# Kernel optimization log

Hardware: AMD Instinct MI355X
Metric: run time of the kernel (lower is better)

Reference implementation:

```python
import jax, jax.numpy as jnp
import numpy as np

N_EMBED = 1024
HEAD_SIZE = 128
B, T = 8, 2048


def setup_inputs() -> dict:
    key = jax.random.key(0)
    kx, kk, kq, kv = jax.random.split(key, 4)
    x = jax.random.normal(kx, (B, T, N_EMBED), dtype=jnp.float32)
    Wk = jax.random.normal(kk, (N_EMBED, HEAD_SIZE), dtype=jnp.float32) * (N_EMBED ** -0.5)
    Wq = jax.random.normal(kq, (N_EMBED, HEAD_SIZE), dtype=jnp.float32) * (N_EMBED ** -0.5)
    Wv = jax.random.normal(kv, (N_EMBED, HEAD_SIZE), dtype=jnp.float32) * (N_EMBED ** -0.5)
    return {"x": x, "Wk": Wk, "Wq": Wq, "Wv": Wv}


def reference(x, Wk, Wq, Wv):
    # x: [B, T, C]; single-head causal attention, dropout rate 0 (identity)
    t = x.shape[1]
    k = jnp.einsum("btc,ch->bth", x, Wk)  # keys
    q = jnp.einsum("btc,ch->bth", x, Wq)  # queries
    v = jnp.einsum("btc,ch->bth", x, Wv)  # values
    scale = k.shape[-1] ** -0.5
    scores = jnp.einsum("bqh,bkh->bqk", q, k) * scale  # [B, T, T]
    causal = jnp.tril(jnp.ones((t, t), dtype=bool))
    scores = jnp.where(causal, scores, -jnp.inf)
    attn = jax.nn.softmax(scores, axis=-1)
    return jnp.einsum("bqk,bkh->bqh", attn, v)
```

## Files before the change

### kernel.cpp

```cpp
#include <hip/hip_runtime.h>
#include <hip/hip_bf16.h>
#include <math.h>

#define B_ 8
#define T_ 2048
#define C_ 1024
#define D_ 128
#define M_ (B_*T_)

typedef __attribute__((ext_vector_type(8))) short short8;
typedef __attribute__((ext_vector_type(4))) float floatx4;
typedef __hip_bfloat16 bf16;

#define QSCALE 0.12751744416218247f

#define GLDS16(gsrc, ldst) \
    __builtin_amdgcn_global_load_lds((const __attribute__((address_space(1))) unsigned int*)(gsrc), \
                                     (__attribute__((address_space(3))) unsigned int*)(ldst), 16, 0, 0)

__global__ __launch_bounds__(256) void cvt_w3_kernel(const float* __restrict__ Wq,
                                                     const float* __restrict__ Wk,
                                                     const float* __restrict__ Wv,
                                                     bf16* __restrict__ Wt2) {
    __shared__ bf16 tl[64][136];
    const int t = threadIdx.x;
    const int kc = blockIdx.x, g = blockIdx.y;
    const int k0 = kc * 64;
    const float* W = (g == 0) ? Wq : (g == 1) ? Wk : Wv;
    {
        int k = t >> 2, n0 = (t & 3) * 32;
        const float* src = W + (size_t)(k0 + k) * 128 + n0;
#pragma unroll
        for (int j = 0; j < 4; ++j) {
            float4 v0 = *(const float4*)(src + j * 8);
            float4 v1 = *(const float4*)(src + j * 8 + 4);
            union { short8 s; __hip_bfloat162 h[4]; } u;
            __hip_bfloat162 h;
            h.x = __float2bfloat16(v0.x); h.y = __float2bfloat16(v0.y); u.h[0] = h;
            h.x = __float2bfloat16(v0.z); h.y = __float2bfloat16(v0.w); u.h[1] = h;
            h.x = __float2bfloat16(v1.x); h.y = __float2bfloat16(v1.y); u.h[2] = h;
            h.x = __float2bfloat16(v1.z); h.y = __float2bfloat16(v1.w); u.h[3] = h;
            *(short8*)&tl[k][n0 + j * 8] = u.s;
        }
    }
    __syncthreads();
    {
#pragma unroll
        for (int j = 0; j < 4; ++j) {
            int cid = t + j * 256;
            int lane = cid & 63, dk = (cid >> 6) & 1, cb = cid >> 7;
            int krow = dk * 32 + (lane >> 4) * 8;
            int ncol = cb * 16 + (lane & 15);
            union { short8 s; bf16 e[8]; } u;
#pragma unroll
            for (int e = 0; e < 8; ++e) u.e[e] = tl[krow + e][ncol];
            bf16* dst = Wt2 + ((((size_t)(g * 8 + cb) * 16 + kc) * 2 + dk) * 64 + lane) * 8;
            *(short8*)dst = u.s;
        }
    }
}

__global__ __launch_bounds__(256, 2) void proj12_kernel(const float* __restrict__ x,
                                                        const bf16* __restrict__ Wt2,
                                                        bf16* __restrict__ Qb,
                                                        bf16* __restrict__ Kb,
                                                        bf16* __restrict__ Vt) {
    __shared__ bf16 smem[21504];
    bf16* wlds = smem;
    bf16* xlds = smem + 12288;
    const int t = threadIdx.x;
    const int wave = t >> 6, lane = t & 63;
    const int quad = lane >> 4, l15 = lane & 15;
    const int wr = wave >> 1, wc = wave & 1;
    const int phys = blockIdx.x;
    const int lb = (phys & 7) * 64 + (phys >> 3);
    const int rt = lb >> 1, cg = lb & 1;
    const int row0 = rt * 64;
    const int xrow = t >> 2, xc16 = (t & 3) * 16;
    const float* xbase = x + (size_t)(row0 + xrow) * 1024 + xc16;

    floatx4 acc[2][6];
#pragma unroll
    for (int m = 0; m < 2; ++m)
#pragma unroll
        for (int n = 0; n < 6; ++n) acc[m][n] = (floatx4)0.0f;

    float4 xf[4];

#pragma unroll
    for (int j = 0; j < 4; ++j) xf[j] = *(const float4*)(xbase + j * 4);
    {
        union { short8 s[2]; __hip_bfloat162 h[8]; } u;
        __hip_bfloat162 h;
#pragma unroll
        for (int j = 0; j < 4; ++j) {
            h.x = __float2bfloat16(xf[j].x); h.y = __float2bfloat16(xf[j].y); u.h[2 * j] = h;
            h.x = __float2bfloat16(xf[j].z); h.y = __float2bfloat16(xf[j].w); u.h[2 * j + 1] = h;
        }
        *(short8*)&xlds[xrow * 72 + xc16] = u.s[0];
        *(short8*)&xlds[xrow * 72 + xc16 + 8] = u.s[1];
    }
#pragma unroll
    for (int j = 0; j < 4; ++j) xf[j] = *(const float4*)(xbase + 64 + j * 4);

    for (int kc = 0; kc < 16; ++kc) {
        __syncthreads();
#pragma unroll
        for (int j = 0; j < 6; ++j) {
            const int s = j * 4 + wave;
            const int cbg = cg * 12 + (s >> 1);
            const size_t chunk = ((size_t)(cbg * 16 + kc) * 2 + (s & 1));
            GLDS16(Wt2 + chunk * 512 + lane * 8, wlds + s * 512);
        }
        if (kc < 15) {
            union { short8 s[2]; __hip_bfloat162 h[8]; } u;
            __hip_bfloat162 h;
#pragma unroll
            for (int j = 0; j < 4; ++j) {
                h.x = __float2bfloat16(xf[j].x); h.y = __float2bfloat16(xf[j].y); u.h[2 * j] = h;
                h.x = __float2bfloat16(xf[j].z); h.y = __float2bfloat16(xf[j].w); u.h[2 * j + 1] = h;
            }
            bf16* xb = xlds + ((kc + 1) & 1) * 4608;
            *(short8*)&xb[xrow * 72 + xc16] = u.s[0];
            *(short8*)&xb[xrow * 72 + xc16 + 8] = u.s[1];
        }
        __syncthreads();
        if (kc < 14) {
#pragma unroll
            for (int j = 0; j < 4; ++j) xf[j] = *(const float4*)(xbase + (kc + 2) * 64 + j * 4);
        }
        const bf16* xb = xlds + (kc & 1) * 4608;
#pragma unroll
        for (int dk = 0; dk < 2; ++dk) {
            short8 af[2], bf[6];
#pragma unroll
            for (int m = 0; m < 2; ++m)
                af[m] = *(const short8*)&xb[(wr * 32 + m * 16 + l15) * 72 + dk * 32 + quad * 8];
#pragma unroll
            for (int n = 0; n < 6; ++n)
                bf[n] = *(const short8*)&wlds[(size_t)((wc * 6 + n) * 2 + dk) * 512 + lane * 8];
#pragma unroll
            for (int m = 0; m < 2; ++m)
#pragma unroll
                for (int n = 0; n < 6; ++n)
                    acc[m][n] = __builtin_amdgcn_mfma_f32_16x16x32_bf16(af[m], bf[n], acc[m][n], 0, 0, 0);
        }
    }

    __syncthreads();
    bf16* vtl = smem;
#pragma unroll
    for (int m = 0; m < 2; ++m)
#pragma unroll
        for (int r = 0; r < 4; ++r) {
            const int tt = wr * 32 + m * 16 + quad * 4 + r;
            const int row = row0 + tt;
#pragma unroll
            for (int n = 0; n < 6; ++n) {
                const int colb = cg * 192 + wc * 96 + n * 16;
                const int g = colb >> 7;
                const int lc = (colb & 127) + l15;
                const float v = acc[m][n][r];
                if (g == 0)      Qb[(size_t)row * 128 + lc] = __float2bfloat16(v * QSCALE);
                else if (g == 1) Kb[(size_t)row * 128 + lc] = __float2bfloat16(v);
                else             vtl[tt * 137 + lc] = __float2bfloat16(v);
            }
        }
    if (cg == 1) {
        __syncthreads();
        int d = t >> 1, toff = (t & 1) * 32;
        union { short8 s[4]; bf16 e[32]; } u;
#pragma unroll
        for (int i = 0; i < 32; ++i) u.e[i] = vtl[(toff + i) * 137 + d];
        int bb = row0 >> 11, t0 = row0 & 2047;
        bf16* dst = Vt + (size_t)(bb * D_ + d) * T_ + t0 + toff;
#pragma unroll
        for (int j = 0; j < 4; ++j) *(short8*)(dst + j * 8) = u.s[j];
    }
}

__global__ __launch_bounds__(256, 3) void flash_fm2_kernel(const bf16* __restrict__ Qb,
                                                           const bf16* __restrict__ Kb,
                                                           const bf16* __restrict__ Vt,
                                                           float* __restrict__ out,
                                                           bf16* __restrict__ Opart,
                                                           float* __restrict__ Lpart) {
    const int tile = blockIdx.x, seg = blockIdx.y, b = blockIdx.z;
    const int keys_total = (tile + 1) * 64;
    const int nseg = (keys_total + 255) >> 8;
    if (seg >= nseg) return;

    __shared__ bf16 lds_k[64][136];
    __shared__ bf16 lds_v[128][72];
    __shared__ bf16 lds_p[4][16][72];
    const int t = threadIdx.x;
    const int wave = t >> 6, lane = t & 63;
    const int quad = lane >> 4, l15 = lane & 15;
    const int q0 = tile * 64;
    const int k_start = seg << 8;
    const int k_end = min(k_start + 256, keys_total);
    const int nch = (k_end - k_start) >> 6;

    short8 qf[4];
    {
        int qm = q0 + wave * 16 + l15;
#pragma unroll
        for (int dk = 0; dk < 4; ++dk)
            qf[dk] = *(const short8*)(Qb + (size_t)(b * T_ + qm) * 128 + dk * 32 + quad * 8);
    }

    short8 kreg[4], vreg[4];
    {
        const int k0 = k_start;
#pragma unroll
        for (int j = 0; j < 4; ++j) {
            int c = t + j * 256;
            { int r = c >> 4, co = (c & 15) * 8;
              kreg[j] = *(const short8*)(Kb + (size_t)(b * T_ + k0 + r) * 128 + co); }
            { int d = c >> 3, co = (c & 7) * 8;
              vreg[j] = *(const short8*)(Vt + (size_t)b * (D_ * T_) + d * T_ + k0 + co); }
        }
    }

    floatx4 o_acc[8];
#pragma unroll
    for (int i = 0; i < 8; ++i) o_acc[i] = (floatx4)0.0f;
    float lp[4] = {0.f, 0.f, 0.f, 0.f};
    const int qrow = q0 + wave * 16 + quad * 4;

    for (int ch = 0; ch < nch; ++ch) {
        const int k0 = k_start + (ch << 6);
        __syncthreads();
#pragma unroll
        for (int j = 0; j < 4; ++j) {
            int c = t + j * 256;
            { int r = c >> 4, co = (c & 15) * 8; *(short8*)&lds_k[r][co] = kreg[j]; }
            { int d = c >> 3, co = (c & 7) * 8;  *(short8*)&lds_v[d][co] = vreg[j]; }
        }
        if (ch + 1 < nch) {
            const int kn = k0 + 64;
#pragma unroll
            for (int j = 0; j < 4; ++j) {
                int c = t + j * 256;
                { int r = c >> 4, co = (c & 15) * 8;
                  kreg[j] = *(const short8*)(Kb + (size_t)(b * T_ + kn + r) * 128 + co); }
                { int d = c >> 3, co = (c & 7) * 8;
                  vreg[j] = *(const short8*)(Vt + (size_t)b * (D_ * T_) + d * T_ + kn + co); }
            }
        }
        __syncthreads();

        floatx4 s[4];
#pragma unroll
        for (int nt = 0; nt < 4; ++nt) s[nt] = (floatx4)0.0f;
#pragma unroll
        for (int dk = 0; dk < 4; ++dk)
#pragma unroll
            for (int nt = 0; nt < 4; ++nt) {
                short8 kb = *(const short8*)&lds_k[nt * 16 + l15][dk * 32 + quad * 8];
                s[nt] = __builtin_amdgcn_mfma_f32_16x16x32_bf16(qf[dk], kb, s[nt], 0, 0, 0);
            }

        float sv[4][4];
#pragma unroll
        for (int nt = 0; nt < 4; ++nt)
#pragma unroll
            for (int r = 0; r < 4; ++r) sv[nt][r] = s[nt][r];

        if (k0 + 63 > q0) {
#pragma unroll
            for (int nt = 0; nt < 4; ++nt) {
                int key = k0 + nt * 16 + l15;
#pragma unroll
                for (int r = 0; r < 4; ++r)
                    if (key > qrow + r) sv[nt][r] = -1e30f;
            }
        }

#pragma unroll
        for (int nt = 0; nt < 4; ++nt)
#pragma unroll
            for (int r = 0; r < 4; ++r) sv[nt][r] = exp2f(sv[nt][r]);
#pragma unroll
        for (int r = 0; r < 4; ++r)
            lp[r] += (sv[0][r] + sv[1][r]) + (sv[2][r] + sv[3][r]);

#pragma unroll
        for (int nt = 0; nt < 4; ++nt)
#pragma unroll
            for (int r = 0; r < 4; ++r)
                lds_p[wave][quad * 4 + r][nt * 16 + l15] = __float2bfloat16(sv[nt][r]);
        short8 pa0 = *(const short8*)&lds_p[wave][l15][quad * 8];
        short8 pa1 = *(const short8*)&lds_p[wave][l15][32 + quad * 8];

#pragma unroll
        for (int nt = 0; nt < 8; ++nt) {
            short8 vb0 = *(const short8*)&lds_v[nt * 16 + l15][quad * 8];
            short8 vb1 = *(const short8*)&lds_v[nt * 16 + l15][32 + quad * 8];
            o_acc[nt] = __builtin_amdgcn_mfma_f32_16x16x32_bf16(pa0, vb0, o_acc[nt], 0, 0, 0);
            o_acc[nt] = __builtin_amdgcn_mfma_f32_16x16x32_bf16(pa1, vb1, o_acc[nt], 0, 0, 0);
        }
    }

    float l_i[4];
#pragma unroll
    for (int r = 0; r < 4; ++r) {
        float v = lp[r];
        v += __shfl_xor(v, 1);
        v += __shfl_xor(v, 2);
        v += __shfl_xor(v, 4);
        v += __shfl_xor(v, 8);
        l_i[r] = v;
    }

    const int lrow = wave * 16 + quad * 4;
    if (nseg == 1) {
        float inv_l[4];
#pragma unroll
        for (int r = 0; r < 4; ++r) inv_l[r] = 1.0f / l_i[r];
#pragma unroll
        for (int f = 0; f < 8; ++f)
#pragma unroll
            for (int r = 0; r < 4; ++r)
                out[(size_t)(b * T_ + qrow + r) * 128 + f * 16 + l15] = o_acc[f][r] * inv_l[r];
    } else {
        int pre = 0;
        for (int u = 4; u < tile; ++u) pre += (u + 4) >> 2;
        const size_t slot = (size_t)b * 140 + pre + seg;
        bf16* ob = Opart + slot * (64 * 128);
#pragma unroll
        for (int f = 0; f < 8; ++f)
#pragma unroll
            for (int r = 0; r < 4; ++r)
                ob[(size_t)(lrow + r) * 128 + f * 16 + l15] = __float2bfloat16(o_acc[f][r]);
        if (l15 == 0) {
#pragma unroll
            for (int r = 0; r < 4; ++r)
                Lpart[slot * 64 + lrow + r] = l_i[r];
        }
    }
}

__global__ __launch_bounds__(256) void combine4_kernel(const bf16* __restrict__ Opart,
                                                       const float* __restrict__ Lpart,
                                                       float* __restrict__ out) {
    const int tile = blockIdx.x + 4, b = blockIdx.y;
    const int nseg = (tile + 4) >> 2;
    int pre = 0;
    for (int u = 4; u < tile; ++u) pre += (u + 4) >> 2;
    const size_t slot0 = (size_t)b * 140 + pre;
    const int t = threadIdx.x;
    const int row = t >> 2, c0 = (t & 3) * 32;

    float lsum = 0.f;
    for (int j = 0; j < nseg; ++j) lsum += Lpart[(slot0 + j) * 64 + row];

    float acc[32];
#pragma unroll
    for (int i = 0; i < 32; ++i) acc[i] = 0.f;
    for (int j = 0; j < nseg; ++j) {
        const bf16* src = Opart + (slot0 + j) * (64 * 128) + (size_t)row * 128 + c0;
#pragma unroll
        for (int u = 0; u < 4; ++u) {
            short8 v8 = *(const short8*)(src + u * 8);
#pragma unroll
            for (int e = 0; e < 8; ++e) {
                union { unsigned int u32; float f; } cv;
                cv.u32 = ((unsigned int)(unsigned short)v8[e]) << 16;
                acc[u * 8 + e] += cv.f;
            }
        }
    }
    float inv = 1.0f / lsum;
    float* dst = out + (size_t)(b * T_ + tile * 64 + row) * 128 + c0;
#pragma unroll
    for (int i = 0; i < 32; ++i) dst[i] = acc[i] * inv;
}

extern "C" void kernel_launch(void* const* d_in, const int* in_sizes, int n_in,
                              void* d_out, int out_size, void* d_ws, size_t ws_size,
                              hipStream_t stream) {
    const float* x  = (const float*)d_in[0];
    const float* Wk = (const float*)d_in[1];
    const float* Wq = (const float*)d_in[2];
    const float* Wv = (const float*)d_in[3];
    float* out = (float*)d_out;

    char* ws = (char*)d_ws;
    bf16*  Wt2   = (bf16*)ws;
    bf16*  Qb    = (bf16*)(ws + 786432);
    bf16*  Kb    = (bf16*)(ws + 4980736);
    bf16*  Vt    = (bf16*)(ws + 9175040);
    bf16*  Opart = (bf16*)(ws + 13369344);
    float* Lpart = (float*)(ws + 31719424);

    cvt_w3_kernel<<<dim3(16, 3), 256, 0, stream>>>(Wq, Wk, Wv, Wt2);
    proj12_kernel<<<512, 256, 0, stream>>>(x, Wt2, Qb, Kb, Vt);
    flash_fm2_kernel<<<dim3(32, 8, B_), 256, 0, stream>>>(Qb, Kb, Vt, out, Opart, Lpart);
    combine4_kernel<<<dim3(28, B_), 256, 0, stream>>>(Opart, Lpart, out);
}
```

Measured before the change: 86.08 us.

## Stream fp32 x tiles into LDS via global_load_lds and convert at fragment load

```diff
diff --git a/kernel.cpp b/kernel.cpp
--- a/kernel.cpp
+++ b/kernel.cpp
@@ -60,14 +60,13 @@
     }
 }
 
-__global__ __launch_bounds__(256, 2) void proj12_kernel(const float* __restrict__ x,
+__global__ __launch_bounds__(256, 2) void proj13_kernel(const float* __restrict__ x,
                                                         const bf16* __restrict__ Wt2,
                                                         bf16* __restrict__ Qb,
                                                         bf16* __restrict__ Kb,
                                                         bf16* __restrict__ Vt) {
-    __shared__ bf16 smem[21504];
-    bf16* wlds = smem;
-    bf16* xlds = smem + 12288;
+    __shared__ char smem[57344];
+    bf16* wlds = (bf16*)smem;
     const int t = threadIdx.x;
     const int wave = t >> 6, lane = t & 63;
     const int quad = lane >> 4, l15 = lane & 15;
@@ -76,8 +75,20 @@
     const int lb = (phys & 7) * 64 + (phys >> 3);
     const int rt = lb >> 1, cg = lb & 1;
     const int row0 = rt * 64;
-    const int xrow = t >> 2, xc16 = (t & 3) * 16;
-    const float* xbase = x + (size_t)(row0 + xrow) * 1024 + xc16;
+
+    const float* xsrc[4];
+#pragma unroll
+    for (int j = 0; j < 4; ++j)
+        xsrc[j] = x + (size_t)(row0 + (wave * 4 + j) * 4 + quad) * 1024
+                    + 4 * ((lane & 15) ^ ((j & 1) * 4 + quad));
+
+    const bf16* wsrc[6];
+#pragma unroll
+    for (int j = 0; j < 6; ++j) {
+        const int s = j * 4 + wave;
+        const int chunkbase = (cg * 12 + (s >> 1)) * 32 + (s & 1);
+        wsrc[j] = Wt2 + (size_t)chunkbase * 512 + lane * 8;
+    }
 
     floatx4 acc[2][6];
 #pragma unroll
@@ -85,70 +96,57 @@
 #pragma unroll
         for (int n = 0; n < 6; ++n) acc[m][n] = (floatx4)0.0f;
 
-    float4 xf[4];
-
-#pragma unroll
-    for (int j = 0; j < 4; ++j) xf[j] = *(const float4*)(xbase + j * 4);
-    {
-        union { short8 s[2]; __hip_bfloat162 h[8]; } u;
-        __hip_bfloat162 h;
-#pragma unroll
-        for (int j = 0; j < 4; ++j) {
-            h.x = __float2bfloat16(xf[j].x); h.y = __float2bfloat16(xf[j].y); u.h[2 * j] = h;
-            h.x = __float2bfloat16(xf[j].z); h.y = __float2bfloat16(xf[j].w); u.h[2 * j + 1] = h;
-        }
-        *(short8*)&xlds[xrow * 72 + xc16] = u.s[0];
-        *(short8*)&xlds[xrow * 72 + xc16 + 8] = u.s[1];
-    }
-#pragma unroll
-    for (int j = 0; j < 4; ++j) xf[j] = *(const float4*)(xbase + 64 + j * 4);
+#pragma unroll
+    for (int j = 0; j < 4; ++j)
+        GLDS16(xsrc[j], smem + 24576 + (wave * 4 + j) * 1024);
 
     for (int kc = 0; kc < 16; ++kc) {
         __syncthreads();
 #pragma unroll
         for (int j = 0; j < 6; ++j) {
             const int s = j * 4 + wave;
-            const int cbg = cg * 12 + (s >> 1);
-            const size_t chunk = ((size_t)(cbg * 16 + kc) * 2 + (s & 1));
-            GLDS16(Wt2 + chunk * 512 + lane * 8, wlds + s * 512);
-        }
+            GLDS16(wsrc[j] + kc * 1024, smem + s * 1024);
+        }
+        __syncthreads();
         if (kc < 15) {
-            union { short8 s[2]; __hip_bfloat162 h[8]; } u;
-            __hip_bfloat162 h;
-#pragma unroll
-            for (int j = 0; j < 4; ++j) {
-                h.x = __float2bfloat16(xf[j].x); h.y = __float2bfloat16(xf[j].y); u.h[2 * j] = h;
-                h.x = __float2bfloat16(xf[j].z); h.y = __float2bfloat16(xf[j].w); u.h[2 * j + 1] = h;
-            }
-            bf16* xb = xlds + ((kc + 1) & 1) * 4608;
-            *(short8*)&xb[xrow * 72 + xc16] = u.s[0];
-            *(short8*)&xb[xrow * 72 + xc16 + 8] = u.s[1];
-        }
-        __syncthreads();
-        if (kc < 14) {
-#pragma unroll
-            for (int j = 0; j < 4; ++j) xf[j] = *(const float4*)(xbase + (kc + 2) * 64 + j * 4);
-        }
-        const bf16* xb = xlds + (kc & 1) * 4608;
+            char* xd = smem + 24576 + ((kc + 1) & 1) * 16384;
+#pragma unroll
+            for (int j = 0; j < 4; ++j)
+                GLDS16(xsrc[j] + (kc + 1) * 64, xd + (wave * 4 + j) * 1024);
+        }
+        const float* xb = (const float*)(smem + 24576 + (kc & 1) * 16384);
 #pragma unroll
         for (int dk = 0; dk < 2; ++dk) {
-            short8 af[2], bf[6];
+            short8 af[2], bff[6];
+#pragma unroll
+            for (int m = 0; m < 2; ++m) {
+                const int r = wr * 32 + m * 16 + l15;
+                const int p0 = (dk * 32 + quad * 8) ^ ((l15 & 7) * 4);
+                float4 a0 = *(const float4*)(xb + r * 64 + p0);
+                float4 a1 = *(const float4*)(xb + r * 64 + (p0 ^ 4));
+                union { short8 s; __hip_bfloat162 h[4]; } u;
+                __hip_bfloat162 hh;
+                hh.x = __float2bfloat16(a0.x); hh.y = __float2bfloat16(a0.y); u.h[0] = hh;
+                hh.x = __float2bfloat16(a0.z); hh.y = __float2bfloat16(a0.w); u.h[1] = hh;
+                hh.x = __float2bfloat16(a1.x); hh.y = __float2bfloat16(a1.y); u.h[2] = hh;
+                hh.x = __float2bfloat16(a1.z); hh.y = __float2bfloat16(a1.w); u.h[3] = hh;
+                af[m] = u.s;
+            }
+#pragma unroll
+            for (int n = 0; n < 6; ++n) {
+                const int c = wc * 6 + n;
+                bff[n] = *(const short8*)(wlds + (size_t)(c * 2 + dk) * 512 + lane * 8);
+            }
 #pragma unroll
             for (int m = 0; m < 2; ++m)
-                af[m] = *(const short8*)&xb[(wr * 32 + m * 16 + l15) * 72 + dk * 32 + quad * 8];
-#pragma unroll
-            for (int n = 0; n < 6; ++n)
-                bf[n] = *(const short8*)&wlds[(size_t)((wc * 6 + n) * 2 + dk) * 512 + lane * 8];
-#pragma unroll
-            for (int m = 0; m < 2; ++m)
 #pragma unroll
                 for (int n = 0; n < 6; ++n)
-                    acc[m][n] = __builtin_amdgcn_mfma_f32_16x16x32_bf16(af[m], bf[n], acc[m][n], 0, 0, 0);
+                    acc[m][n] = __builtin_amdgcn_mfma_f32_16x16x32_bf16(af[m], bff[n], acc[m][n], 0, 0, 0);
         }
     }
 
     __syncthreads();
-    bf16* vtl = smem;
+    bf16* vtl = (bf16*)smem;
 #pragma unroll
     for (int m = 0; m < 2; ++m)
 #pragma unroll
@@ -395,7 +393,7 @@
     float* Lpart = (float*)(ws + 31719424);
 
     cvt_w3_kernel<<<dim3(16, 3), 256, 0, stream>>>(Wq, Wk, Wv, Wt2);
-    proj12_kernel<<<512, 256, 0, stream>>>(x, Wt2, Qb, Kb, Vt);
+    proj13_kernel<<<512, 256, 0, stream>>>(x, Wt2, Qb, Kb, Vt);
     flash_fm2_kernel<<<dim3(32, 8, B_), 256, 0, stream>>>(Qb, Kb, Vt, out, Opart, Lpart);
     combine4_kernel<<<dim3(28, B_), 256, 0, stream>>>(Opart, Lpart, out);
 }
```

Result: faster. 84.33 us (-2.0%).
